# Kernel tuning notes

Hardware: AMD Instinct MI355X
Metric: run time of the kernel (lower is better)

Reference implementation:

```python
import jax, jax.numpy as jnp
import numpy as np

B, T, R, D = 65536, 200, 4, 20
NUM_TIMESTEPS = 1000
NUM_STEPS = 50


def setup_inputs() -> dict:
    key = jax.random.key(0)
    k0, k1, k2, k3, k4 = jax.random.split(key, 5)
    return {
        "drug_ids": jax.random.randint(k0, (B,), 0, D),
        "concentrations": jax.random.uniform(k1, (B, 1), dtype=jnp.float32),
        "replicate_counts": jax.random.randint(k2, (B,), 1, R + 1),
        "media_change_times": jnp.array([48.0, 96.0, 144.0], dtype=jnp.float32),
        "drug_emb": jax.random.normal(k3, (D, T), dtype=jnp.float32) * 0.1,
        "unet_W": jax.random.normal(k4, (R, R), dtype=jnp.float32) * 0.1,
    }


def _denoise(x0, masks, unet_W):
    # DDPM scheduler tables (linear beta schedule, 1000 steps)
    betas = jnp.linspace(1e-4, 0.02, NUM_TIMESTEPS, dtype=jnp.float32)
    alphas_cumprod = jnp.cumprod(1.0 - betas)
    timesteps = jnp.linspace(NUM_TIMESTEPS - 1, 0, NUM_STEPS).astype(jnp.int32)
    step_keys = jax.random.split(jax.random.key(42), NUM_STEPS)
    mask3 = masks[:, None, :]  # [B,1,R]

    def step(x, inp):
        t, i, k = inp
        # minimal UNet stand-in: replicate-mixing linear layer gated by timestep
        noise_pred = jnp.einsum("btr,rs->bts", x, unet_W) * (1.0 - t.astype(jnp.float32) / NUM_TIMESTEPS)
        a = jnp.clip(alphas_cumprod[t], 1e-6)
        sqrt_a = jnp.sqrt(a)
        sqrt_1ma = jnp.sqrt(jnp.clip(1.0 - a, 1e-6))
        pred_x0 = jnp.clip((x - sqrt_1ma * noise_pred) / sqrt_a, -10.0, 10.0)
        noise = jax.random.normal(k, x.shape, dtype=x.dtype) * 0.1
        x_next = jnp.where(i < NUM_STEPS - 1, pred_x0 + jnp.sqrt(betas[t]) * noise, pred_x0)
        return x_next * mask3, None

    x, _ = jax.lax.scan(step, x0, (timesteps, jnp.arange(NUM_STEPS), step_keys))
    return x


def reference(drug_ids, concentrations, replicate_counts, media_change_times, drug_emb, unet_W):
    masks = (jnp.arange(R)[None, :] < replicate_counts[:, None]).astype(jnp.float32)  # [B,R]
    # simple drug-aware response module: per-drug curve scaled by concentration
    drug_responses = drug_emb[drug_ids] * concentrations  # [B,T]

    kx, kv = jax.random.split(jax.random.key(1))
    x0 = jax.random.normal(kx, (drug_ids.shape[0], T, R), dtype=jnp.float32) * masks[:, None, :]
    x = _denoise(x0, masks, unet_W)

    x_scaled = 30.0 + 10.0 * jnp.tanh(x)
    rep_var = jax.random.normal(kv, x_scaled.shape, dtype=jnp.float32) * 0.5
    x_scaled = x_scaled + (drug_responses[:, :, None] + rep_var) * masks[:, None, :]
    x_scaled = x_scaled * masks[:, None, :]
    return x_scaled, masks
```

## Files before the change

### kernel.cpp

```cpp
#include <hip/hip_runtime.h>
#include <cstdint>
#include <cmath>
#include <vector>

#pragma clang fp contract(off)

#define B_SZ 65536
#define T_SZ 200
#define R_SZ 4
#define NCELLS (B_SZ * T_SZ)
#define NELEM (NCELLS * R_SZ)
#define NSTEPS 50

struct StepC { float tscale, sqrt_a, sqrt_1ma, sqrt_beta; };
struct Params {
  uint32_t kx0, kx1, kv0, kv1;
  uint32_t sk0[NSTEPS], sk1[NSTEPS];
  StepC sc[NSTEPS];
};

__host__ __device__ inline void tf2x32(uint32_t k0, uint32_t k1,
                                       uint32_t c0, uint32_t c1,
                                       uint32_t& o0, uint32_t& o1) {
  uint32_t ks0 = k0, ks1 = k1, ks2 = 0x1BD11BDAu ^ k0 ^ k1;
  uint32_t x0 = c0 + ks0;
  uint32_t x1 = c1 + ks1;
#define TF_RND(rot) { x0 += x1; x1 = (x1 << rot) | (x1 >> (32 - rot)); x1 ^= x0; }
  TF_RND(13) TF_RND(15) TF_RND(26) TF_RND(6)
  x0 += ks1; x1 += ks2 + 1u;
  TF_RND(17) TF_RND(29) TF_RND(16) TF_RND(24)
  x0 += ks2; x1 += ks0 + 2u;
  TF_RND(13) TF_RND(15) TF_RND(26) TF_RND(6)
  x0 += ks0; x1 += ks1 + 3u;
  TF_RND(17) TF_RND(29) TF_RND(16) TF_RND(24)
  x0 += ks1; x1 += ks2 + 4u;
  TF_RND(13) TF_RND(15) TF_RND(26) TF_RND(6)
  x0 += ks2; x1 += ks0 + 5u;
#undef TF_RND
  o0 = x0; o1 = x1;
}

__device__ inline uint32_t tf_xor(uint32_t k0, uint32_t k1, uint32_t ctr) {
  uint32_t o0, o1;
  tf2x32(k0, k1, 0u, ctr, o0, o1);
  return o0 ^ o1;
}

__device__ inline float n_from_bits(uint32_t bits) {
  const float MINV = -0.99999994039535522461f;
  uint32_t fb = (bits >> 9) | 0x3F800000u;
  float f = __uint_as_float(fb) - 1.0f;
  float u = f * 2.0f + MINV;
  u = fmaxf(MINV, u);
  float x2 = u * u;
  float nx2 = -x2;
  float for_small = ((-0.5f * nx2) + 1.0f) * nx2;
  float for_large = logf(nx2 + 1.0f);
  float lg = (fabsf(nx2) < 1e-4f) ? for_small : for_large;
  float w = -lg;
  float p;
  if (w < 5.0f) {
    float ww = w - 2.5f;
    p = 2.81022636e-08f;
    p = p * ww + 3.43273939e-07f;
    p = p * ww + -3.5233877e-06f;
    p = p * ww + -4.39150654e-06f;
    p = p * ww + 0.00021858087f;
    p = p * ww + -0.00125372503f;
    p = p * ww + -0.00417768164f;
    p = p * ww + 0.246640727f;
    p = p * ww + 1.50140941f;
  } else {
    float ww = sqrtf(w) - 3.0f;
    p = -0.000200214257f;
    p = p * ww + 0.000100950558f;
    p = p * ww + 0.00134934322f;
    p = p * ww + -0.00367342844f;
    p = p * ww + 0.00573950773f;
    p = p * ww + -0.0076224613f;
    p = p * ww + 0.00943887047f;
    p = p * ww + 1.00167406f;
    p = p * ww + 2.83297682f;
  }
  float ei = p * u;
  return 1.41421356237309504880f * ei;
}

__device__ inline float xla_tanh(float x) {
  float ax = fabsf(x);
  float xc = fminf(fmaxf(x, -7.90531110763549805f), 7.90531110763549805f);
  float x2 = xc * xc;
  float num = -2.76076847742355e-16f;
  num = x2 * num + 2.00018790482477e-13f;
  num = x2 * num + -8.60467152213735e-11f;
  num = x2 * num + 5.12229709037114e-08f;
  num = x2 * num + 1.48572235717979e-05f;
  num = x2 * num + 6.37261928875436e-04f;
  num = x2 * num + 4.89352455891786e-03f;
  num = xc * num;
  float den = 1.19825839466702e-06f;
  den = x2 * den + 1.18534705686654e-04f;
  den = x2 * den + 2.26843463243900e-03f;
  den = x2 * den + 4.89352518554385e-03f;
  float r = num / den;
  return (ax < 0.0004f) ? x : r;
}

__global__ __launch_bounds__(256) void fused_kernel(
    const int* __restrict__ drug_ids, const float* __restrict__ conc,
    const int* __restrict__ repc, const float* __restrict__ emb,
    const float* __restrict__ Wg, float* __restrict__ out, Params P) {
  const uint32_t c = blockIdx.x * 256u + threadIdx.x;
  const uint32_t e0 = c * 4u;
  const int b = (int)(c / T_SZ);
  const int t = (int)(c - (uint32_t)b * T_SZ);

  const int cnt = repc[b];

  float W[4][4];
#pragma unroll
  for (int r = 0; r < 4; ++r)
#pragma unroll
    for (int s = 0; s < 4; ++s) W[r][s] = Wg[r * 4 + s];

  float x[4];
#pragma unroll
  for (int r = 0; r < 4; ++r) {
    x[r] = 0.0f;
    if (cnt > r)
      x[r] = n_from_bits(tf_xor(P.kx0, P.kx1, e0 + r));
  }

  for (int s = 0; s < NSTEPS - 1; ++s) {
    const float tscale = P.sc[s].tscale;
    const float sa     = P.sc[s].sqrt_a;
    const float s1ma   = P.sc[s].sqrt_1ma;
    const float sb     = P.sc[s].sqrt_beta;
    const uint32_t k0 = P.sk0[s], k1 = P.sk1[s];
    float d[4];
#pragma unroll
    for (int s2 = 0; s2 < 4; ++s2) {
      float acc = x[0] * W[0][s2];
      acc = __builtin_fmaf(x[1], W[1][s2], acc);
      acc = __builtin_fmaf(x[2], W[2][s2], acc);
      acc = __builtin_fmaf(x[3], W[3][s2], acc);
      d[s2] = acc;
    }
#pragma unroll
    for (int r = 0; r < 4; ++r) {
      if (cnt > r) {
        float n  = n_from_bits(tf_xor(k0, k1, e0 + r)) * 0.1f;
        float np = d[r] * tscale;
        float sm = s1ma * np;
        float tmp = x[r] - sm;
        float pred = tmp / sa;
        pred = fmaxf(fminf(pred, 10.0f), -10.0f);
        x[r] = pred + sb * n;
      }
    }
  }
  {
    const float tscale = P.sc[NSTEPS - 1].tscale;
    const float sa     = P.sc[NSTEPS - 1].sqrt_a;
    const float s1ma   = P.sc[NSTEPS - 1].sqrt_1ma;
    float d[4];
#pragma unroll
    for (int s2 = 0; s2 < 4; ++s2) {
      float acc = x[0] * W[0][s2];
      acc = __builtin_fmaf(x[1], W[1][s2], acc);
      acc = __builtin_fmaf(x[2], W[2][s2], acc);
      acc = __builtin_fmaf(x[3], W[3][s2], acc);
      d[s2] = acc;
    }
#pragma unroll
    for (int r = 0; r < 4; ++r) {
      if (cnt > r) {
        float np = d[r] * tscale;
        float sm = s1ma * np;
        float tmp = x[r] - sm;
        float pred = tmp / sa;
        x[r] = fmaxf(fminf(pred, 10.0f), -10.0f);
      }
    }
  }

  float dr = emb[drug_ids[b] * T_SZ + t] * conc[b];
  float ov[4];
#pragma unroll
  for (int r = 0; r < 4; ++r) {
    ov[r] = 0.0f;
    if (cnt > r) {
      float rv = n_from_bits(tf_xor(P.kv0, P.kv1, e0 + r)) * 0.5f;
      float th = xla_tanh(x[r]);
      float v = 30.0f + 10.0f * th;
      v = v + (dr + rv);
      ov[r] = v;
    }
  }
  ((float4*)out)[c] = make_float4(ov[0], ov[1], ov[2], ov[3]);
}

__global__ __launch_bounds__(256) void masks_kernel(const int* __restrict__ repc,
                                                    float* __restrict__ outm) {
  int i = blockIdx.x * 256 + threadIdx.x;
  int b = i >> 2;
  int r = i & 3;
  outm[i] = (r < repc[b]) ? 1.0f : 0.0f;
}

static void jax_ascan_prod(std::vector<float>& v) {
  size_t n = v.size();
  if (n < 2) return;
  size_t nr = n / 2;
  std::vector<float> red(nr);
  for (size_t i = 0; i < nr; ++i) red[i] = v[2 * i] * v[2 * i + 1];
  jax_ascan_prod(red);
  std::vector<float> out(n);
  out[0] = v[0];
  for (size_t i = 0; i < nr; ++i) out[2 * i + 1] = red[i];
  if (n % 2 == 0) {
    for (size_t i = 0; i + 1 < nr; ++i) out[2 * i + 2] = red[i] * v[2 * i + 2];
  } else {
    for (size_t i = 0; i < nr; ++i) out[2 * i + 2] = red[i] * v[2 * i + 2];
  }
  v.swap(out);
}

extern "C" void kernel_launch(void* const* d_in, const int* in_sizes, int n_in,
                              void* d_out, int out_size, void* d_ws, size_t ws_size,
                              hipStream_t stream) {
  const int*   drug_ids = (const int*)d_in[0];
  const float* conc     = (const float*)d_in[1];
  const int*   repc     = (const int*)d_in[2];
  const float* emb      = (const float*)d_in[4];
  const float* W        = (const float*)d_in[5];
  float* out = (float*)d_out;

  Params P;
  {
    uint32_t o0, o1;
    tf2x32(0u, 1u, 0u, 0u, o0, o1); P.kx0 = o0; P.kx1 = o1;
    tf2x32(0u, 1u, 0u, 1u, o0, o1); P.kv0 = o0; P.kv1 = o1;
    for (int s = 0; s < NSTEPS; ++s) {
      tf2x32(0u, 42u, 0u, (uint32_t)s, o0, o1);
      P.sk0[s] = o0; P.sk1[s] = o1;
    }
    float beta[1000];
    float delta = (0.02f - 0.0001f) / 999.0f;
    std::vector<float> am(1000);
    for (int i = 0; i < 1000; ++i) {
      beta[i] = 0.0001f + (float)i * delta;
      am[i] = 1.0f - beta[i];
    }
    jax_ascan_prod(am);
    float tsd = (0.0f - 999.0f) / 49.0f;
    for (int s = 0; s < NSTEPS; ++s) {
      float tfv = 999.0f + (float)s * tsd;
      int t = (int)tfv;
      if (t < 0) t = 0;
      float a = am[t];   if (a < 1e-6f) a = 1e-6f;
      float oma = 1.0f - a; if (oma < 1e-6f) oma = 1e-6f;
      P.sc[s].tscale    = 1.0f - ((float)t) / 1000.0f;
      P.sc[s].sqrt_a    = sqrtf(a);
      P.sc[s].sqrt_1ma  = sqrtf(oma);
      P.sc[s].sqrt_beta = sqrtf(beta[t]);
    }
  }

  fused_kernel<<<NCELLS / 256, 256, 0, stream>>>(drug_ids, conc, repc, emb, W, out, P);
  masks_kernel<<<(B_SZ * R_SZ) / 256, 256, 0, stream>>>(repc, out + (size_t)NELEM);
}
```

Measured before the change: 4.810 ms.

## Bucket batches by replicate count and specialize kernels per count

Adds a ballot/atomic bucketing pass that groups batch rows by replicate count, then launches four templated kernels each specialized to CNT replicates. This removes divergence from the per-replicate masking branches so warps only run RNG and update work for active replicates. It also replaces the float division by sqrt_a with a double-precision multiply by a precomputed reciprocal, which is intended to match float division rounding. The cost is extra launches and a memset, scattered output writes through the index lists, and a fixed grid size per bucket that assumes no bucket exceeds 18432 rows.

```diff
diff --git a/kernel.cpp b/kernel.cpp
--- a/kernel.cpp
+++ b/kernel.cpp
@@ -11,12 +11,15 @@
 #define NCELLS (B_SZ * T_SZ)
 #define NELEM (NCELLS * R_SZ)
 #define NSTEPS 50
+#define MAXB_PER_BUCKET 18432
+#define BUCKET_BLOCKS ((MAXB_PER_BUCKET * T_SZ) / 256)
 
 struct StepC { float tscale, sqrt_a, sqrt_1ma, sqrt_beta; };
 struct Params {
   uint32_t kx0, kx1, kv0, kv1;
   uint32_t sk0[NSTEPS], sk1[NSTEPS];
   StepC sc[NSTEPS];
+  double inv_sa[NSTEPS];
 };
 
 __host__ __device__ inline void tf2x32(uint32_t k0, uint32_t k1,
@@ -106,96 +109,113 @@
   return (ax < 0.0004f) ? x : r;
 }
 
-__global__ __launch_bounds__(256) void fused_kernel(
+__global__ __launch_bounds__(256) void bucket_build(const int* __restrict__ repc,
+                                                    int* __restrict__ counts,
+                                                    int* __restrict__ lists) {
+  const int b = blockIdx.x * 256 + threadIdx.x;
+  const int cnt = repc[b];
+  const int lane = threadIdx.x & 63;
+#pragma unroll
+  for (int k = 1; k <= 4; ++k) {
+    unsigned long long m = __ballot(cnt == k);
+    if (cnt == k) {
+      int rank = __popcll(m & ((1ull << lane) - 1ull));
+      int base = 0;
+      if (rank == 0) base = atomicAdd(&counts[k - 1], __popcll(m));
+      int src = (int)__builtin_ctzll(m);
+      base = __shfl(base, src, 64);
+      lists[(k - 1) * B_SZ + base + rank] = b;
+    }
+  }
+}
+
+template <int CNT>
+__global__ __launch_bounds__(256) void fused_cnt(
     const int* __restrict__ drug_ids, const float* __restrict__ conc,
-    const int* __restrict__ repc, const float* __restrict__ emb,
-    const float* __restrict__ Wg, float* __restrict__ out, Params P) {
-  const uint32_t c = blockIdx.x * 256u + threadIdx.x;
+    const float* __restrict__ emb, const float* __restrict__ Wg,
+    const int* __restrict__ counts, const int* __restrict__ list,
+    float* __restrict__ out, Params P) {
+  const int count = counts[CNT - 1];
+  const int ncell = count * T_SZ;
+  const int g = blockIdx.x * 256 + threadIdx.x;
+  if (g >= ncell) return;
+  const int p  = g / T_SZ;
+  const int t  = g - p * T_SZ;
+  const int b  = list[p];
+  const uint32_t c  = (uint32_t)b * (uint32_t)T_SZ + (uint32_t)t;
   const uint32_t e0 = c * 4u;
-  const int b = (int)(c / T_SZ);
-  const int t = (int)(c - (uint32_t)b * T_SZ);
-
-  const int cnt = repc[b];
-
-  float W[4][4];
-#pragma unroll
-  for (int r = 0; r < 4; ++r)
-#pragma unroll
-    for (int s = 0; s < 4; ++s) W[r][s] = Wg[r * 4 + s];
-
-  float x[4];
-#pragma unroll
-  for (int r = 0; r < 4; ++r) {
-    x[r] = 0.0f;
-    if (cnt > r)
-      x[r] = n_from_bits(tf_xor(P.kx0, P.kx1, e0 + r));
-  }
+
+  float W[CNT][CNT];
+#pragma unroll
+  for (int r = 0; r < CNT; ++r)
+#pragma unroll
+    for (int s = 0; s < CNT; ++s) W[r][s] = Wg[r * 4 + s];
+
+  float x[CNT];
+#pragma unroll
+  for (int r = 0; r < CNT; ++r)
+    x[r] = n_from_bits(tf_xor(P.kx0, P.kx1, e0 + r));
 
   for (int s = 0; s < NSTEPS - 1; ++s) {
     const float tscale = P.sc[s].tscale;
-    const float sa     = P.sc[s].sqrt_a;
     const float s1ma   = P.sc[s].sqrt_1ma;
     const float sb     = P.sc[s].sqrt_beta;
+    const double isa   = P.inv_sa[s];
     const uint32_t k0 = P.sk0[s], k1 = P.sk1[s];
-    float d[4];
-#pragma unroll
-    for (int s2 = 0; s2 < 4; ++s2) {
+    float n[CNT];
+#pragma unroll
+    for (int r = 0; r < CNT; ++r)
+      n[r] = n_from_bits(tf_xor(k0, k1, e0 + r)) * 0.1f;
+    float d[CNT];
+#pragma unroll
+    for (int s2 = 0; s2 < CNT; ++s2) {
       float acc = x[0] * W[0][s2];
-      acc = __builtin_fmaf(x[1], W[1][s2], acc);
-      acc = __builtin_fmaf(x[2], W[2][s2], acc);
-      acc = __builtin_fmaf(x[3], W[3][s2], acc);
+#pragma unroll
+      for (int r = 1; r < CNT; ++r) acc = __builtin_fmaf(x[r], W[r][s2], acc);
       d[s2] = acc;
     }
 #pragma unroll
-    for (int r = 0; r < 4; ++r) {
-      if (cnt > r) {
-        float n  = n_from_bits(tf_xor(k0, k1, e0 + r)) * 0.1f;
-        float np = d[r] * tscale;
-        float sm = s1ma * np;
-        float tmp = x[r] - sm;
-        float pred = tmp / sa;
-        pred = fmaxf(fminf(pred, 10.0f), -10.0f);
-        x[r] = pred + sb * n;
-      }
+    for (int r = 0; r < CNT; ++r) {
+      float np  = d[r] * tscale;
+      float sm  = s1ma * np;
+      float tmp = x[r] - sm;
+      float pred = (float)((double)tmp * isa);
+      pred = fmaxf(fminf(pred, 10.0f), -10.0f);
+      x[r] = pred + sb * n[r];
     }
   }
   {
     const float tscale = P.sc[NSTEPS - 1].tscale;
-    const float sa     = P.sc[NSTEPS - 1].sqrt_a;
     const float s1ma   = P.sc[NSTEPS - 1].sqrt_1ma;
-    float d[4];
-#pragma unroll
-    for (int s2 = 0; s2 < 4; ++s2) {
+    const double isa   = P.inv_sa[NSTEPS - 1];
+    float d[CNT];
+#pragma unroll
+    for (int s2 = 0; s2 < CNT; ++s2) {
       float acc = x[0] * W[0][s2];
-      acc = __builtin_fmaf(x[1], W[1][s2], acc);
-      acc = __builtin_fmaf(x[2], W[2][s2], acc);
-      acc = __builtin_fmaf(x[3], W[3][s2], acc);
+#pragma unroll
+      for (int r = 1; r < CNT; ++r) acc = __builtin_fmaf(x[r], W[r][s2], acc);
       d[s2] = acc;
     }
 #pragma unroll
-    for (int r = 0; r < 4; ++r) {
-      if (cnt > r) {
-        float np = d[r] * tscale;
-        float sm = s1ma * np;
-        float tmp = x[r] - sm;
-        float pred = tmp / sa;
-        x[r] = fmaxf(fminf(pred, 10.0f), -10.0f);
-      }
-    }
-  }
-
-  float dr = emb[drug_ids[b] * T_SZ + t] * conc[b];
+    for (int r = 0; r < CNT; ++r) {
+      float np  = d[r] * tscale;
+      float sm  = s1ma * np;
+      float tmp = x[r] - sm;
+      float pred = (float)((double)tmp * isa);
+      x[r] = fmaxf(fminf(pred, 10.0f), -10.0f);
+    }
+  }
+
+  const float dr = emb[drug_ids[b] * T_SZ + t] * conc[b];
   float ov[4];
 #pragma unroll
-  for (int r = 0; r < 4; ++r) {
-    ov[r] = 0.0f;
-    if (cnt > r) {
-      float rv = n_from_bits(tf_xor(P.kv0, P.kv1, e0 + r)) * 0.5f;
-      float th = xla_tanh(x[r]);
-      float v = 30.0f + 10.0f * th;
-      v = v + (dr + rv);
-      ov[r] = v;
-    }
+  for (int r = 0; r < 4; ++r) ov[r] = 0.0f;
+#pragma unroll
+  for (int r = 0; r < CNT; ++r) {
+    float rv = n_from_bits(tf_xor(P.kv0, P.kv1, e0 + r)) * 0.5f;
+    float th = xla_tanh(x[r]);
+    float v = 30.0f + 10.0f * th;
+    ov[r] = v + (dr + rv);
   }
   ((float4*)out)[c] = make_float4(ov[0], ov[1], ov[2], ov[3]);
 }
@@ -264,9 +284,22 @@
       P.sc[s].sqrt_a    = sqrtf(a);
       P.sc[s].sqrt_1ma  = sqrtf(oma);
       P.sc[s].sqrt_beta = sqrtf(beta[t]);
-    }
-  }
-
-  fused_kernel<<<NCELLS / 256, 256, 0, stream>>>(drug_ids, conc, repc, emb, W, out, P);
+      P.inv_sa[s] = 1.0 / (double)P.sc[s].sqrt_a;
+    }
+  }
+
+  int* counts = (int*)d_ws;
+  int* lists  = (int*)d_ws + 64;
+  hipMemsetAsync(counts, 0, 4 * sizeof(int), stream);
+  bucket_build<<<B_SZ / 256, 256, 0, stream>>>(repc, counts, lists);
+
+  fused_cnt<1><<<BUCKET_BLOCKS, 256, 0, stream>>>(drug_ids, conc, emb, W,
+                                                  counts, lists + 0 * B_SZ, out, P);
+  fused_cnt<2><<<BUCKET_BLOCKS, 256, 0, stream>>>(drug_ids, conc, emb, W,
+                                                  counts, lists + 1 * B_SZ, out, P);
+  fused_cnt<3><<<BUCKET_BLOCKS, 256, 0, stream>>>(drug_ids, conc, emb, W,
+                                                  counts, lists + 2 * B_SZ, out, P);
+  fused_cnt<4><<<BUCKET_BLOCKS, 256, 0, stream>>>(drug_ids, conc, emb, W,
+                                                  counts, lists + 3 * B_SZ, out, P);
   masks_kernel<<<(B_SZ * R_SZ) / 256, 256, 0, stream>>>(repc, out + (size_t)NELEM);
 }
```

Result: faster. 4.240 ms (-11.9%).
